# Optimization experiments

Hardware: AMD Instinct MI355X
Metric: run time of the kernel (lower is better)

Reference implementation:

```python
import jax, jax.numpy as jnp
import numpy as np

B, S, H = 32, 2048, 1024

def setup_inputs() -> dict:
    key = jax.random.key(0)
    ks = jax.random.split(key, 8)
    scale = 1.0 / np.sqrt(H)
    return {
        "query": jax.random.normal(ks[0], (B, H), jnp.float32),
        "keys": jax.random.normal(ks[1], (B, S, H), jnp.float32),
        "Wa_w": jax.random.uniform(ks[2], (H, H), jnp.float32, -scale, scale),
        "Wa_b": jax.random.uniform(ks[3], (H,), jnp.float32, -scale, scale),
        "Ua_w": jax.random.uniform(ks[4], (H, H), jnp.float32, -scale, scale),
        "Ua_b": jax.random.uniform(ks[5], (H,), jnp.float32, -scale, scale),
        "Va_w": jax.random.uniform(ks[6], (1, H), jnp.float32, -scale, scale),
        "Va_b": jax.random.uniform(ks[7], (1,), jnp.float32, -scale, scale),
    }

def reference(query, keys, Wa_w, Wa_b, Ua_w, Ua_b, Va_w, Va_b):
    # q_proj: [B, H]; k_proj: [B, S, H]  (torch Linear: x @ W^T + b)
    q_proj = query @ Wa_w.T + Wa_b
    k_proj = jnp.einsum("bsh,gh->bsg", keys, Ua_w) + Ua_b
    # scores: [B, S, 1] via thin Va projection of tanh-combined features
    scores = jnp.tanh(q_proj[:, None, :] + k_proj) @ Va_w.T + Va_b
    weights = jax.nn.softmax(scores, axis=1)            # [B, S, 1]
    context = jnp.einsum("bsx,bsh->bxh", weights, keys)  # [B, 1, H]
    return context, weights[:, :, 0]
```

## Files before the change

### kernel.cpp

```cpp
#include <hip/hip_runtime.h>
#include <hip/hip_bf16.h>
#include <stdint.h>

#define B_ 32
#define S_ 2048
#define H_ 1024

typedef __attribute__((ext_vector_type(8))) short short8;
typedef __attribute__((ext_vector_type(4))) float floatx4;

__device__ inline unsigned short f32_bf16(float f) {
    union { float f; unsigned u; } v; v.f = f;
    unsigned u = v.u;
    u += 0x7fff + ((u >> 16) & 1);
    return (unsigned short)(u >> 16);
}
__device__ inline unsigned pack_bf2(float a, float b) {
    return (unsigned)f32_bf16(a) | ((unsigned)f32_bf16(b) << 16);
}
__device__ inline float bf_lo(unsigned u) { union { unsigned u; float f; } v; v.u = u << 16; return v.f; }
__device__ inline float bf_hi(unsigned u) { union { unsigned u; float f; } v; v.u = u & 0xffff0000u; return v.f; }

__device__ inline float tanh_fast(float x) {
    float e = __expf(2.0f * x);
    return 1.0f - 2.0f / (e + 1.0f);
}

__device__ inline void gld16(const void* g, void* l) {
    __builtin_amdgcn_global_load_lds(
        (const __attribute__((address_space(1))) unsigned int*)g,
        (__attribute__((address_space(3))) unsigned int*)l, 16, 0, 0);
}

#define KCVT_BLOCKS 32768
#define UACVT_BLOCKS 512
#define QP_BLOCKS 64
__global__ void k_prep(const float* __restrict__ keys, unsigned short* __restrict__ keysbf,
                       const float* __restrict__ ua, unsigned short* __restrict__ uab,
                       const float* __restrict__ query, const float* __restrict__ Wa_w,
                       const float* __restrict__ Wa_b, const float* __restrict__ Ua_b,
                       float* __restrict__ qsum) {
    int blk = blockIdx.x, t = threadIdx.x;
    if (blk < KCVT_BLOCKS + UACVT_BLOCKS) {
        const float* src; unsigned short* dst; size_t base;
        if (blk < KCVT_BLOCKS) { src = keys; dst = keysbf; base = (size_t)blk * 2048; }
        else { src = ua; dst = uab; base = (size_t)(blk - KCVT_BLOCKS) * 2048; }
        float4 v0 = *(const float4*)(src + base + t * 4);
        float4 v1 = *(const float4*)(src + base + 1024 + t * 4);
        *(uint2*)(dst + base + t * 4)        = make_uint2(pack_bf2(v0.x, v0.y), pack_bf2(v0.z, v0.w));
        *(uint2*)(dst + base + 1024 + t * 4) = make_uint2(pack_bf2(v1.x, v1.y), pack_bf2(v1.z, v1.w));
    } else {
        __shared__ float qs_l[32][68];
        int g0 = (blk - KCVT_BLOCKS - UACVT_BLOCKS) * 16;
        int r = t >> 4, l = t & 15;
        int g = g0 + r;
        float acc[32];
#pragma unroll
        for (int b = 0; b < 32; ++b) acc[b] = 0.0f;
        int sb = t >> 3, sc = (t & 7) * 8;
        for (int hc = 0; hc < 16; ++hc) {
            __syncthreads();
            float4 v0 = *(const float4*)(query + (size_t)sb * H_ + hc * 64 + sc);
            float4 v1 = *(const float4*)(query + (size_t)sb * H_ + hc * 64 + sc + 4);
            *(float4*)&qs_l[sb][sc]     = v0;
            *(float4*)&qs_l[sb][sc + 4] = v1;
            __syncthreads();
            float4 w = *(const float4*)(Wa_w + (size_t)g * H_ + hc * 64 + l * 4);
#pragma unroll
            for (int b = 0; b < 32; ++b) {
                float4 q4 = *(const float4*)&qs_l[b][l * 4];
                acc[b] += w.x * q4.x + w.y * q4.y + w.z * q4.z + w.w * q4.w;
            }
        }
#pragma unroll
        for (int b = 0; b < 32; ++b) {
            float a = acc[b];
            a += __shfl_xor(a, 1); a += __shfl_xor(a, 2);
            a += __shfl_xor(a, 4); a += __shfl_xor(a, 8);
            acc[b] = a;
        }
        if (l == 0) {
            float bias = Wa_b[g] + Ua_b[g];
#pragma unroll
            for (int b = 0; b < 32; ++b) qsum[b * H_ + g] = acc[b] + bias;
        }
    }
}

#define BM 256
#define BN 256
#define BK 64

#define VMCNT(S) asm volatile("s_waitcnt vmcnt(" S ")" ::: "memory")

#define STAGE_A(SB, h, KO) do {                                                       \
    gld16(pAj[0] + (h) * 64 * H_ + (KO), &Al[(SB) * 16384 + (h) * 8192 + sA]);        \
    gld16(pAj[1] + (h) * 64 * H_ + (KO), &Al[(SB) * 16384 + (h) * 8192 + sA + 512]);  \
} while (0)
#define STAGE_B(SB, h, KO) do {                                                       \
    gld16(pBj[0] + (h) * 32 * H_ + (KO), &Bl[(SB) * 16384 + (h) * 8192 + sA]);        \
    gld16(pBj[1] + (h) * 32 * H_ + (KO), &Bl[(SB) * 16384 + (h) * 8192 + sA + 512]);  \
} while (0)

#define MFMA_BF16 __builtin_amdgcn_mfma_f32_16x16x32_bf16

#define STEP(RB, SB, KO, W1, W2, DOST, DOV4) do {                                      \
               \
    _Pragma("unroll") for (int ii_ = 0; ii_ < 4; ++ii_) {                              \
        af[ii_][0] = *(const short8*)&Al[(RB) + arA + ii_ * 1024 + cs0];               \
        af[ii_][1] = *(const short8*)&Al[(RB) + arA + ii_ * 1024 + cs1]; }             \
    _Pragma("unroll") for (int jj_ = 0; jj_ < 2; ++jj_) {                              \
        bfa[jj_][0] = *(const short8*)&Bl[(RB) + brB + jj_ * 1024 + cs0];              \
        bfa[jj_][1] = *(const short8*)&Bl[(RB) + brB + jj_ * 1024 + cs1]; }            \
    if (DOST) STAGE_A(SB, 0, KO);                                                      \
    __builtin_amdgcn_s_barrier();                                                      \
    __builtin_amdgcn_s_setprio(1);                                                     \
    _Pragma("unroll") for (int ii_ = 0; ii_ < 4; ++ii_)                                \
    _Pragma("unroll") for (int jj_ = 0; jj_ < 2; ++jj_) {                              \
        acc[ii_][jj_] = MFMA_BF16(af[ii_][0], bfa[jj_][0], acc[ii_][jj_], 0, 0, 0);    \
        acc[ii_][jj_] = MFMA_BF16(af[ii_][1], bfa[jj_][1], acc[ii_][jj_], 0, 0, 0); }  \
    __builtin_amdgcn_s_setprio(0);                                                     \
    VMCNT(W1);                                                                         \
    __builtin_amdgcn_s_barrier();                                                      \
                  \
    _Pragma("unroll") for (int jj_ = 0; jj_ < 2; ++jj_) {                              \
        bfb[jj_][0] = *(const short8*)&Bl[(RB) + 8192 + brB + jj_ * 1024 + cs0];       \
        bfb[jj_][1] = *(const short8*)&Bl[(RB) + 8192 + brB + jj_ * 1024 + cs1]; }     \
    if (DOST) STAGE_B(SB, 0, KO);                                                      \
    __builtin_amdgcn_s_barrier();                                                      \
    __builtin_amdgcn_s_setprio(1);                                                     \
    _Pragma("unroll") for (int ii_ = 0; ii_ < 4; ++ii_)                                \
    _Pragma("unroll") for (int jj_ = 0; jj_ < 2; ++jj_) {                              \
        acc[ii_][jj_ + 2] = MFMA_BF16(af[ii_][0], bfb[jj_][0], acc[ii_][jj_ + 2], 0, 0, 0); \
        acc[ii_][jj_ + 2] = MFMA_BF16(af[ii_][1], bfb[jj_][1], acc[ii_][jj_ + 2], 0, 0, 0); } \
    __builtin_amdgcn_s_setprio(0);                                                     \
    VMCNT(W2);                                                                         \
    __builtin_amdgcn_s_barrier();                                                      \
              \
    _Pragma("unroll") for (int ii_ = 0; ii_ < 4; ++ii_) {                              \
        af[ii_][0] = *(const short8*)&Al[(RB) + 8192 + arA + ii_ * 1024 + cs0];        \
        af[ii_][1] = *(const short8*)&Al[(RB) + 8192 + arA + ii_ * 1024 + cs1]; }      \
    if (DOST) STAGE_B(SB, 1, KO);                                                      \
    __builtin_amdgcn_s_barrier();                                                      \
    __builtin_amdgcn_s_setprio(1);                                                     \
    _Pragma("unroll") for (int ii_ = 0; ii_ < 4; ++ii_)                                \
    _Pragma("unroll") for (int jj_ = 0; jj_ < 2; ++jj_) {                              \
        acc[ii_ + 4][jj_] = MFMA_BF16(af[ii_][0], bfa[jj_][0], acc[ii_ + 4][jj_], 0, 0, 0); \
        acc[ii_ + 4][jj_] = MFMA_BF16(af[ii_][1], bfa[jj_][1], acc[ii_ + 4][jj_], 0, 0, 0); } \
    __builtin_amdgcn_s_setprio(0);                                                     \
    __builtin_amdgcn_s_barrier();                                                      \
          \
    if (DOST) STAGE_A(SB, 1, KO);                                                      \
    __builtin_amdgcn_s_barrier();                                                      \
    __builtin_amdgcn_s_setprio(1);                                                     \
    _Pragma("unroll") for (int ii_ = 0; ii_ < 4; ++ii_)                                \
    _Pragma("unroll") for (int jj_ = 0; jj_ < 2; ++jj_) {                              \
        acc[ii_ + 4][jj_ + 2] = MFMA_BF16(af[ii_][0], bfb[jj_][0], acc[ii_ + 4][jj_ + 2], 0, 0, 0); \
        acc[ii_ + 4][jj_ + 2] = MFMA_BF16(af[ii_][1], bfb[jj_][1], acc[ii_ + 4][jj_ + 2], 0, 0, 0); } \
    __builtin_amdgcn_s_setprio(0);                                                     \
    if (DOV4) VMCNT("4");                                                              \
    __builtin_amdgcn_s_barrier();                                                      \
} while (0)

__global__ __launch_bounds__(512, 2) void k_scores(
    const unsigned short* __restrict__ keysbf, const unsigned short* __restrict__ uab,
    const float* __restrict__ qsum, const float* __restrict__ va,
    float* __restrict__ scores_p)
{
    __shared__ unsigned short Al[32768];
    __shared__ unsigned short Bl[32768];

    int bx = blockIdx.x;
    int x  = bx & 7;
    int i  = bx >> 3;
    int tile_m = x * 32 + (i >> 2);
    int nc     = i & 3;
    int m_base = tile_m * BM;
    int b      = m_base >> 11;
    int g0     = nc * BN;

    int tid = threadIdx.x;
    int wid = tid >> 6, lane = tid & 63;
    int wm = wid >> 2, wn = wid & 3;
    int q = lane >> 4, cn = lane & 15;
    int c7 = cn & 7;

    int rl8 = lane >> 3;
    int gcg = (lane & 7) ^ rl8;
    int ch0 = wid * 2;
    const unsigned short* pAj[2];
    const unsigned short* pBj[2];
#pragma unroll
    for (int j = 0; j < 2; ++j) {
        int hlrow = (ch0 + j) * 8 + rl8;
        pAj[j] = keysbf + (size_t)(m_base + (hlrow >> 6) * 128 + (hlrow & 63)) * H_ + gcg * 8;
        pBj[j] = uab    + (size_t)(g0 + (hlrow >> 5) * 64 + (hlrow & 31)) * H_ + gcg * 8;
    }
    int sA = ch0 * 512;

    int arA = wm * 4096 + cn * 64;
    int brB = wn * 2048 + cn * 64;
    int cs0 = (q ^ c7) * 8;
    int cs1 = ((4 + q) ^ c7) * 8;

    floatx4 acc[8][4];
#pragma unroll
    for (int ii = 0; ii < 8; ++ii)
#pragma unroll
        for (int jj = 0; jj < 4; ++jj)
            acc[ii][jj] = (floatx4)(0.0f);

    short8 af[4][2], bfa[2][2], bfb[2][2];

    STAGE_A(0, 0, 0);
    STAGE_B(0, 0, 0);
    STAGE_B(0, 1, 0);
    STAGE_A(0, 1, 0);
    VMCNT("4");
    __builtin_amdgcn_s_barrier();

#pragma unroll 1
    for (int it = 0; it < 7; ++it) {
        int ko = it * 128 + 64;
        STEP(0,     1, ko,      "4", "4", 1, 1);
        STEP(16384, 0, ko + 64, "4", "4", 1, 1);
    }
    STEP(0,     1, 960, "4", "4", 1, 1);
    STEP(16384, 0, 0,   "2", "0", 0, 0);

    float qs[4], vw[4];
#pragma unroll
    for (int jj = 0; jj < 4; ++jj) {
        int g = g0 + wn * 64 + jj * 16 + cn;
        qs[jj] = qsum[b * H_ + g];
        vw[jj] = va[g];
    }
    float* slab = scores_p + (size_t)(wn * 4 + nc) * (B_ * S_) + b * S_;
#pragma unroll
    for (int ii = 0; ii < 8; ++ii) {
        float rs[4] = {0.f, 0.f, 0.f, 0.f};
#pragma unroll
        for (int jj = 0; jj < 4; ++jj) {
#pragma unroll
            for (int r = 0; r < 4; ++r)
                rs[r] += vw[jj] * tanh_fast(qs[jj] + acc[ii][jj][r]);
        }
#pragma unroll
        for (int r = 0; r < 4; ++r) {
            rs[r] += __shfl_xor(rs[r], 1); rs[r] += __shfl_xor(rs[r], 2);
            rs[r] += __shfl_xor(rs[r], 4); rs[r] += __shfl_xor(rs[r], 8);
        }
        if (cn == 0) {
            int msrow = (m_base & (S_ - 1)) + wm * 128 + ii * 16 + q * 4;
            float* sp = slab + msrow;
            sp[0] = rs[0]; sp[1] = rs[1]; sp[2] = rs[2]; sp[3] = rs[3];
        }
    }
}

__global__ void k_softmax(const float* __restrict__ scores_p, float* __restrict__ weights) {
    int b = blockIdx.x;
    int t = threadIdx.x;
    __shared__ float red[4];
    float v[8];
    float mx = -1e30f;
#pragma unroll
    for (int k = 0; k < 8; ++k) {
        int idx = b * S_ + t + k * 256;
        float s = 0.0f;
#pragma unroll
        for (int p = 0; p < 16; ++p) s += scores_p[(size_t)p * (B_ * S_) + idx];
        v[k] = s; mx = fmaxf(mx, s);
    }
    for (int mm = 1; mm < 64; mm <<= 1) mx = fmaxf(mx, __shfl_xor(mx, mm));
    if ((t & 63) == 0) red[t >> 6] = mx;
    __syncthreads();
    mx = fmaxf(fmaxf(red[0], red[1]), fmaxf(red[2], red[3]));
    float sum = 0.0f;
#pragma unroll
    for (int k = 0; k < 8; ++k) { v[k] = __expf(v[k] - mx); sum += v[k]; }
    for (int mm = 1; mm < 64; mm <<= 1) sum += __shfl_xor(sum, mm);
    __syncthreads();
    if ((t & 63) == 0) red[t >> 6] = sum;
    __syncthreads();
    sum = red[0] + red[1] + red[2] + red[3];
    float inv = 1.0f / sum;
#pragma unroll
    for (int k = 0; k < 8; ++k) weights[b * S_ + t + k * 256] = v[k] * inv;
}

__global__ void k_ctx1(const unsigned short* __restrict__ keysbf,
                       const float* __restrict__ weights, float* __restrict__ partial) {
    int blk = blockIdx.x;
    int b = blk >> 5, sc = blk & 31;
    int t = threadIdx.x;
    __shared__ float wl[64];
    if (t < 64) wl[t] = weights[b * S_ + sc * 64 + t];
    __syncthreads();
    const uint4* kp = (const uint4*)(keysbf + (size_t)(b * S_ + sc * 64) * H_);
    int col = t & 127;
    int rp  = t >> 7;
    float a0=0,a1=0,a2=0,a3=0,a4=0,a5=0,a6=0,a7=0;
#pragma unroll 8
    for (int s = rp; s < 64; s += 2) {
        uint4 v = kp[(size_t)s * 128 + col];
        float w = wl[s];
        a0 += w * bf_lo(v.x); a1 += w * bf_hi(v.x);
        a2 += w * bf_lo(v.y); a3 += w * bf_hi(v.y);
        a4 += w * bf_lo(v.z); a5 += w * bf_hi(v.z);
        a6 += w * bf_lo(v.w); a7 += w * bf_hi(v.w);
    }
    float* pp = partial + (size_t)(b * 64 + sc * 2 + rp) * H_ + col * 8;
    float4 o0 = {a0, a1, a2, a3}, o1 = {a4, a5, a6, a7};
    *(float4*)pp = o0;
    *(float4*)(pp + 4) = o1;
}

__global__ void k_ctx2(const float* __restrict__ partial, float* __restrict__ ctx) {
    int b = blockIdx.x;
    int t = threadIdx.x;
    float4 a = {0.f, 0.f, 0.f, 0.f};
#pragma unroll 8
    for (int j = 0; j < 64; ++j) {
        float4 p = *(const float4*)(partial + (size_t)(b * 64 + j) * H_ + t * 4);
        a.x += p.x; a.y += p.y; a.z += p.z; a.w += p.w;
    }
    *(float4*)(ctx + b * H_ + t * 4) = a;
}

extern "C" void kernel_launch(void* const* d_in, const int* in_sizes, int n_in,
                              void* d_out, int out_size, void* d_ws, size_t ws_size,
                              hipStream_t stream) {
    const float* query = (const float*)d_in[0];
    const float* keys  = (const float*)d_in[1];
    const float* Wa_w  = (const float*)d_in[2];
    const float* Wa_b  = (const float*)d_in[3];
    const float* Ua_w  = (const float*)d_in[4];
    const float* Ua_b  = (const float*)d_in[5];
    const float* Va_w  = (const float*)d_in[6];

    float* out     = (float*)d_out;
    float* ctx     = out;
    float* weights = out + B_ * H_;

    char* ws = (char*)d_ws;
    unsigned short* keysbf  = (unsigned short*)ws;
    unsigned short* uab     = (unsigned short*)(ws + 134217728);
    float*          qsum    = (float*)(ws + 134217728 + 2097152);
    float*          scores_p= (float*)(ws + 134217728 + 2097152 + 131072);
    float*          partial = (float*)(ws + 134217728 + 2097152 + 131072 + 4194304);

    k_prep   <<<KCVT_BLOCKS + UACVT_BLOCKS + QP_BLOCKS, 256, 0, stream>>>(
        keys, keysbf, Ua_w, uab, query, Wa_w, Wa_b, Ua_b, qsum);
    k_scores <<<1024, 512, 0, stream>>>(keysbf, uab, qsum, Va_w, scores_p);
    k_softmax<<<B_, 256, 0, stream>>>(scores_p, weights);
    k_ctx1   <<<B_ * 32, 256, 0, stream>>>(keysbf, weights, partial);
    k_ctx2   <<<B_, 256, 0, stream>>>(partial, ctx);
}
```

Before: 605.1 us.

## Restructure GEMM K-loop pipeline to prefetch half-tiles ahead and cut barriers

Reworks the double-buffered LDS pipeline in the scores GEMM. Each step now issues global-to-LDS loads for the second half of the next tile and the first half of the tile after that. The per-step barriers drop from about seven to two. The goal is to cut synchronisation stalls and keep more loads in flight behind the MFMA work. In exchange, the buffer-reuse and hazard ordering becomes harder to reason about, with a risk of LDS write-after-read races.

```diff
diff --git a/kernel.cpp b/kernel.cpp
--- a/kernel.cpp
+++ b/kernel.cpp
@@ -104,62 +104,51 @@
 
 #define MFMA_BF16 __builtin_amdgcn_mfma_f32_16x16x32_bf16
 
-#define STEP(RB, SB, KO, W1, W2, DOST, DOV4) do {                                      \
-               \
+#define STEP(RB, SB1, SB2, KO1, KO2, DOST1, DOST2, DOBAR, WS) do {                     \
+                           \
     _Pragma("unroll") for (int ii_ = 0; ii_ < 4; ++ii_) {                              \
         af[ii_][0] = *(const short8*)&Al[(RB) + arA + ii_ * 1024 + cs0];               \
         af[ii_][1] = *(const short8*)&Al[(RB) + arA + ii_ * 1024 + cs1]; }             \
     _Pragma("unroll") for (int jj_ = 0; jj_ < 2; ++jj_) {                              \
         bfa[jj_][0] = *(const short8*)&Bl[(RB) + brB + jj_ * 1024 + cs0];              \
         bfa[jj_][1] = *(const short8*)&Bl[(RB) + brB + jj_ * 1024 + cs1]; }            \
-    if (DOST) STAGE_A(SB, 0, KO);                                                      \
-    __builtin_amdgcn_s_barrier();                                                      \
+    if (DOST1) { STAGE_B(SB1, 1, KO1); STAGE_A(SB1, 1, KO1); }                         \
     __builtin_amdgcn_s_setprio(1);                                                     \
     _Pragma("unroll") for (int ii_ = 0; ii_ < 4; ++ii_)                                \
     _Pragma("unroll") for (int jj_ = 0; jj_ < 2; ++jj_) {                              \
         acc[ii_][jj_] = MFMA_BF16(af[ii_][0], bfa[jj_][0], acc[ii_][jj_], 0, 0, 0);    \
         acc[ii_][jj_] = MFMA_BF16(af[ii_][1], bfa[jj_][1], acc[ii_][jj_], 0, 0, 0); }  \
     __builtin_amdgcn_s_setprio(0);                                                     \
-    VMCNT(W1);                                                                         \
-    __builtin_amdgcn_s_barrier();                                                      \
-                  \
+                                                  \
     _Pragma("unroll") for (int jj_ = 0; jj_ < 2; ++jj_) {                              \
         bfb[jj_][0] = *(const short8*)&Bl[(RB) + 8192 + brB + jj_ * 1024 + cs0];       \
         bfb[jj_][1] = *(const short8*)&Bl[(RB) + 8192 + brB + jj_ * 1024 + cs1]; }     \
-    if (DOST) STAGE_B(SB, 0, KO);                                                      \
-    __builtin_amdgcn_s_barrier();                                                      \
     __builtin_amdgcn_s_setprio(1);                                                     \
     _Pragma("unroll") for (int ii_ = 0; ii_ < 4; ++ii_)                                \
     _Pragma("unroll") for (int jj_ = 0; jj_ < 2; ++jj_) {                              \
         acc[ii_][jj_ + 2] = MFMA_BF16(af[ii_][0], bfb[jj_][0], acc[ii_][jj_ + 2], 0, 0, 0); \
         acc[ii_][jj_ + 2] = MFMA_BF16(af[ii_][1], bfb[jj_][1], acc[ii_][jj_ + 2], 0, 0, 0); } \
     __builtin_amdgcn_s_setprio(0);                                                     \
-    VMCNT(W2);                                                                         \
-    __builtin_amdgcn_s_barrier();                                                      \
-              \
+                                   \
     _Pragma("unroll") for (int ii_ = 0; ii_ < 4; ++ii_) {                              \
         af[ii_][0] = *(const short8*)&Al[(RB) + 8192 + arA + ii_ * 1024 + cs0];        \
         af[ii_][1] = *(const short8*)&Al[(RB) + 8192 + arA + ii_ * 1024 + cs1]; }      \
-    if (DOST) STAGE_B(SB, 1, KO);                                                      \
-    __builtin_amdgcn_s_barrier();                                                      \
     __builtin_amdgcn_s_setprio(1);                                                     \
     _Pragma("unroll") for (int ii_ = 0; ii_ < 4; ++ii_)                                \
     _Pragma("unroll") for (int jj_ = 0; jj_ < 2; ++jj_) {                              \
         acc[ii_ + 4][jj_] = MFMA_BF16(af[ii_][0], bfa[jj_][0], acc[ii_ + 4][jj_], 0, 0, 0); \
         acc[ii_ + 4][jj_] = MFMA_BF16(af[ii_][1], bfa[jj_][1], acc[ii_ + 4][jj_], 0, 0, 0); } \
     __builtin_amdgcn_s_setprio(0);                                                     \
-    __builtin_amdgcn_s_barrier();                                                      \
-          \
-    if (DOST) STAGE_A(SB, 1, KO);                                                      \
-    __builtin_amdgcn_s_barrier();                                                      \
+    if (DOBAR) __builtin_amdgcn_s_barrier();                                           \
+                  \
+    if (DOST2) { STAGE_A(SB2, 0, KO2); STAGE_B(SB2, 0, KO2); }                         \
     __builtin_amdgcn_s_setprio(1);                                                     \
     _Pragma("unroll") for (int ii_ = 0; ii_ < 4; ++ii_)                                \
     _Pragma("unroll") for (int jj_ = 0; jj_ < 2; ++jj_) {                              \
         acc[ii_ + 4][jj_ + 2] = MFMA_BF16(af[ii_][0], bfb[jj_][0], acc[ii_ + 4][jj_ + 2], 0, 0, 0); \
         acc[ii_ + 4][jj_ + 2] = MFMA_BF16(af[ii_][1], bfb[jj_][1], acc[ii_ + 4][jj_ + 2], 0, 0, 0); } \
     __builtin_amdgcn_s_setprio(0);                                                     \
-    if (DOV4) VMCNT("4");                                                              \
-    __builtin_amdgcn_s_barrier();                                                      \
+    if (DOBAR) { VMCNT(WS); __builtin_amdgcn_s_barrier(); }                            \
 } while (0)
 
 __global__ __launch_bounds__(512, 2) void k_scores(
@@ -212,21 +201,20 @@
 
     short8 af[4][2], bfa[2][2], bfb[2][2];
 
-    STAGE_A(0, 0, 0);
-    STAGE_B(0, 0, 0);
-    STAGE_B(0, 1, 0);
-    STAGE_A(0, 1, 0);
+    STAGE_A(0, 0, 0);  STAGE_B(0, 0, 0);
+    STAGE_B(0, 1, 0);  STAGE_A(0, 1, 0);
+    STAGE_A(1, 0, 64); STAGE_B(1, 0, 64);
     VMCNT("4");
     __builtin_amdgcn_s_barrier();
 
 #pragma unroll 1
     for (int it = 0; it < 7; ++it) {
-        int ko = it * 128 + 64;
-        STEP(0,     1, ko,      "4", "4", 1, 1);
-        STEP(16384, 0, ko + 64, "4", "4", 1, 1);
-    }
-    STEP(0,     1, 960, "4", "4", 1, 1);
-    STEP(16384, 0, 0,   "2", "0", 0, 0);
+        int t2 = it * 2;
+        STEP(0,     1, 0, (t2 + 1) * 64, (t2 + 2) * 64, 1, 1, 1, "4");
+        STEP(16384, 0, 1, (t2 + 2) * 64, (t2 + 3) * 64, 1, 1, 1, "4");
+    }
+    STEP(0,     1, 0, 960, 0, 1, 0, 1, "0");
+    STEP(16384, 0, 1, 0,   0, 0, 0, 0, "0");
 
     float qs[4], vw[4];
 #pragma unroll
```

Result: no change. 598.8 us (-1.1%).
